# Kernel optimization log

Measured on AMD Instinct MI355X. Metric: run time of the kernel, lower is better.

The kernel has to match this reference:

```python
import jax, jax.numpy as jnp
import numpy as np

DIM = 192
T, H, W = 6, 8, 8
NH = 6
HD = DIM // NH
HW = H * W
N = T * HW
SCALE = HD ** (-0.5)
B_ = 128


def _sine_pos_enc():
    # Faithful port of get_sine_position_encoding(window_size[1:], dim // 2).
    npf = DIM // 2
    ones = jnp.ones((1, H, W), jnp.float32)
    y_embed = jnp.cumsum(ones, axis=1)
    x_embed = jnp.cumsum(ones, axis=2)
    two_pi = 2.0 * np.pi
    y_embed = y_embed / (y_embed[:, -1:, :] + 1e-6) * two_pi
    x_embed = x_embed / (x_embed[:, :, -1:] + 1e-6) * two_pi
    dim_t = jnp.arange(npf, dtype=jnp.float32)
    dim_t = 10000.0 ** (2.0 * jnp.floor(dim_t / 2.0) / npf)
    pos_x = x_embed[:, :, :, None] / dim_t
    pos_y = y_embed[:, :, :, None] / dim_t
    pos_x = jnp.stack((jnp.sin(pos_x[..., 0::2]), jnp.cos(pos_x[..., 1::2])), axis=4).reshape(1, H, W, npf)
    pos_y = jnp.stack((jnp.sin(pos_y[..., 0::2]), jnp.cos(pos_y[..., 1::2])), axis=4).reshape(1, H, W, npf)
    pos = jnp.concatenate((pos_y, pos_x), axis=3)  # (1, H, W, DIM)
    return pos.reshape(1, HW, DIM)


def setup_inputs() -> dict:
    key = jax.random.key(0)
    ks = jax.random.split(key, 6)
    s = 0.02
    return {
        "x": jax.random.normal(ks[0], (B_, N, DIM), jnp.float32),
        "Wqkv": jax.random.normal(ks[1], (3 * DIM, DIM), jnp.float32) * s,
        "Wproj": jax.random.normal(ks[2], (DIM, 2 * DIM), jnp.float32) * s,
        "bproj": jnp.zeros((DIM,), jnp.float32),
        "gamma": jnp.ones((DIM,), jnp.float32),
        "beta": jnp.zeros((DIM,), jnp.float32),
        "W1": jax.random.normal(ks[3], (DIM, DIM), jnp.float32) * s,
        "b1": jnp.zeros((DIM,), jnp.float32),
        "W2": jax.random.normal(ks[4], (DIM, DIM), jnp.float32) * s,
        "b2": jnp.zeros((DIM,), jnp.float32),
    }


def reference(x, Wqkv, Wproj, bproj, gamma, beta, W1, b1, W2, b2):
    b = x.shape[0]
    pos = jnp.tile(_sine_pos_enc(), (1, T, 1))  # (1, N, DIM)
    qkv = (x + pos) @ Wqkv.T                      # (b, N, 3*DIM)
    qkv = qkv.reshape(b, N, 3, NH, HD).transpose(2, 0, 3, 1, 4)
    # temporal chunks: (b, NH, T, HW, HD)
    q = qkv[0].reshape(b, NH, T, HW, HD)
    k = qkv[1].reshape(b, NH, T, HW, HD)
    v = qkv[2].reshape(b, NH, T, HW, HD)
    # all T x T cross-frame attention pairs at once
    scores = jnp.einsum('bhind,bhjmd->ijbhnm', q * SCALE, k)  # (T,T,b,NH,HW,HW)
    attn = jax.nn.softmax(scores, axis=-1)
    o = jnp.einsum('ijbhnm,bhjmd->ijbnhd', attn, v).reshape(T, T, b, HW, DIM)
    # Faithful to torch's x.view(-1, B_, HW, C): raw reinterpretation, not a transpose.
    x_tmp = x.reshape(T, b, HW, DIM)
    xi = jnp.broadcast_to(x_tmp[:, None], (T, T, b, HW, DIM))
    x_att = jnp.concatenate((o, xi), axis=-1)     # (T,T,b,HW,2*DIM)
    y = x_att @ Wproj.T + bproj
    mu = jnp.mean(y, axis=-1, keepdims=True)
    var = jnp.var(y, axis=-1, keepdims=True)
    y = (y - mu) / jnp.sqrt(var + 1e-5) * gamma + beta
    y = jax.nn.gelu(y @ W1.T + b1, approximate=False) @ W2.T + b2
    acc = jnp.sum(y, axis=1)                       # sum over j -> (T,b,HW,DIM)
    x_out = x + acc.transpose(1, 0, 2, 3).reshape(b, N, DIM) / T
    return jnp.concatenate((x, x_out), axis=-1)
```

## Files before the change

### kernel.cpp

```cpp
#include <hip/hip_runtime.h>
#include <cmath>

#define TT   6
#define NB   128
#define DIM  192
#define SCALE 0.17677669529663687f

typedef __attribute__((ext_vector_type(8))) short v8s;
typedef __attribute__((ext_vector_type(4))) float v4f;

__device__ __forceinline__ short f2bf(float f) {
  union { float f; unsigned u; } v; v.f = f;
  unsigned r = v.u + 0x7fffu + ((v.u >> 16) & 1u);
  return (short)(r >> 16);
}

__global__ void prep_kernel(const float* __restrict__ Wqkv, const float* __restrict__ Wproj,
                            const float* __restrict__ W1, const float* __restrict__ W2,
                            short* __restrict__ dWqkv, short* __restrict__ dWproj,
                            short* __restrict__ dW1, short* __restrict__ dW2,
                            float* __restrict__ pos) {
  int idx = blockIdx.x * 256 + threadIdx.x;
  const float* src = nullptr; short* dst = nullptr; int off = 0;
  if (idx < 27648)      { src = Wqkv;  dst = dWqkv;  off = idx; }
  else if (idx < 46080) { src = Wproj; dst = dWproj; off = idx - 27648; }
  else if (idx < 55296) { src = W1;    dst = dW1;    off = idx - 46080; }
  else if (idx < 64512) { src = W2;    dst = dW2;    off = idx - 55296; }
  else if (idx < 67584) {
    int p0 = (idx - 64512) * 4;
    float4 r;
    float* rp = (float*)&r;
#pragma unroll
    for (int jj = 0; jj < 4; jj++) {
      int p = p0 + jj;
      int row = p / 192, c = p - row * 192;
      int e  = (c < 96) ? (row >> 3) : (row & 7);
      int cc = (c < 96) ? c : c - 96;
      int m = cc >> 1;
      float embed = (float)(e + 1) * (6.283185307179586f / 8.000001f);
      float dt = powf(10000.0f, (float)m * (1.0f / 48.0f));
      float ang = embed / dt;
      rp[jj] = (cc & 1) ? cosf(ang) : sinf(ang);
    }
    *(float4*)(pos + p0) = r;
    return;
  } else return;
  const float* s = src + off * 4;
  short4 r;
  r.x = f2bf(s[0]); r.y = f2bf(s[1]); r.z = f2bf(s[2]); r.w = f2bf(s[3]);
  *(short4*)(dst + off * 4) = r;
}

__global__ __launch_bounds__(256) void qkv_kernel(
    const float* __restrict__ x, const float* __restrict__ pos,
    const short* __restrict__ Wqkv_bf,
    short* __restrict__ Qb, short* __restrict__ Kb, short* __restrict__ Vtb) {
  __shared__ short XP[64 * 200];
  int bid = blockIdx.x;
  int xcd = bid & 7, idx = bid >> 3;
  int bq = idx / TT;
  int b = xcd * 16 + bq, t = idx - bq * TT;
  int tid = threadIdx.x, w = tid >> 6, lane = tid & 63;
  int l15 = lane & 15, quad = lane >> 4;
  const float* xrow = x + (size_t)(b * (TT * 64) + t * 64) * DIM;
  for (int c = tid; c < 64 * 24; c += 256) {
    int row = c / 24, col8 = (c - (c / 24) * 24) * 8;
    const float* xs = xrow + row * DIM + col8;
    const float* pp = pos + row * DIM + col8;
    v8s r8;
#pragma unroll
    for (int jj = 0; jj < 8; jj++) r8[jj] = f2bf(xs[jj] + pp[jj]);
    *(v8s*)(XP + row * 200 + col8) = r8;
  }
  __syncthreads();
  const v4f vzero = {0.f, 0.f, 0.f, 0.f};
  size_t obase = (size_t)(b * TT + t) * 64 * DIM;
#pragma unroll
  for (int cti = 0; cti < 9; cti++) {
    int r0 = w * 144 + cti * 16;
    v4f acc[4] = {vzero, vzero, vzero, vzero};
#pragma unroll
    for (int ks = 0; ks < 6; ks++) {
      v8s a = *(const v8s*)(Wqkv_bf + (size_t)(r0 + l15) * 192 + ks * 32 + quad * 8);
#pragma unroll
      for (int nt = 0; nt < 4; nt++) {
        v8s bb = *(const v8s*)(XP + (nt * 16 + l15) * 200 + ks * 32 + quad * 8);
        acc[nt] = __builtin_amdgcn_mfma_f32_16x16x32_bf16(a, bb, acc[nt], 0, 0, 0);
      }
    }
    int R = r0 + quad * 4;
#pragma unroll
    for (int nt = 0; nt < 4; nt++) {
      int hw = nt * 16 + l15;
      if (R < 192) {
        short4 s;
        s.x = f2bf(acc[nt][0] * SCALE); s.y = f2bf(acc[nt][1] * SCALE);
        s.z = f2bf(acc[nt][2] * SCALE); s.w = f2bf(acc[nt][3] * SCALE);
        *(short4*)(Qb + obase + (size_t)hw * 192 + R) = s;
      } else if (R < 384) {
        short4 s;
        s.x = f2bf(acc[nt][0]); s.y = f2bf(acc[nt][1]);
        s.z = f2bf(acc[nt][2]); s.w = f2bf(acc[nt][3]);
        *(short4*)(Kb + obase + (size_t)hw * 192 + (R - 192)) = s;
      } else {
#pragma unroll
        for (int r = 0; r < 4; r++)
          Vtb[obase + (size_t)(R - 384 + r) * 64 + hw] = f2bf(acc[nt][r]);
      }
    }
  }
}

__global__ __launch_bounds__(512, 6) void fused_all(
    const float* __restrict__ x,
    const short* __restrict__ Qb, const short* __restrict__ Kb,
    const short* __restrict__ Vtb,
    const short* __restrict__ Wproj_bf, const short* __restrict__ W1_bf,
    const short* __restrict__ W2_bf,
    const float* __restrict__ bproj, const float* __restrict__ gamma,
    const float* __restrict__ beta, const float* __restrict__ b1,
    const float* __restrict__ b2,
    float* __restrict__ out) {
  __shared__ short SP[64 * 200];
  __shared__ short XI[64 * 200];
  __shared__ float LNp[64][4][2];

  int bid = blockIdx.x;
  int xcd = bid & 7, idx6 = bid >> 3;
  int bq = idx6 / TT;
  int b = xcd * 16 + bq, i = idx6 - bq * TT;

  int tid = threadIdx.x, w = tid >> 6, lane = tid & 63;
  int l15 = lane & 15, quad = lane >> 4;
  int wc = w & 3, wh = w >> 2;
  int cb = wc * 48;
  const v4f vzero = {0.f, 0.f, 0.f, 0.f};

  const float* xi = x + (size_t)(i * NB + b) * 64 * DIM;
  for (int c = tid; c < 64 * 24; c += 512) {
    int row = c / 24, col8 = (c - (c / 24) * 24) * 8;
    const float* xs = xi + row * DIM + col8;
    v8s r8;
#pragma unroll
    for (int jj = 0; jj < 8; jj++) r8[jj] = f2bf(xs[jj]);
    *(v8s*)(XI + row * 200 + col8) = r8;
  }

  const short* Qi = Qb + (size_t)(b * TT + i) * 64 * DIM;
  v8s qa[3];
#pragma unroll
  for (int hh = 0; hh < 3; hh++)
    qa[hh] = *(const v8s*)(Qi + (size_t)(wc * 16 + l15) * 192 + (wh * 3 + hh) * 32 + quad * 8);

  v4f acc[3][2];
#pragma unroll
  for (int cti = 0; cti < 3; cti++)
#pragma unroll
    for (int nt = 0; nt < 2; nt++) acc[cti][nt] = vzero;

  __syncthreads();

  int srcA = l15 + ((lane & 16) << 1);
  int srcB = srcA + 16;
  bool hiq = (lane & 32) != 0;

  for (int j = 0; j < TT; j++) {
    __syncthreads();
    const short* Kj = Kb + (size_t)(b * TT + j) * 64 * DIM;
    const short* Vj = Vtb + (size_t)(b * TT + j) * 64 * DIM;

#pragma unroll
    for (int hh = 0; hh < 3; hh++) {
      int h = wh * 3 + hh;
      v4f S[4];
#pragma unroll
      for (int cta = 0; cta < 4; cta++) {
        v8s akq = *(const v8s*)(Kj + (size_t)(cta * 16 + l15) * 192 + h * 32 + quad * 8);
        S[cta] = __builtin_amdgcn_mfma_f32_16x16x32_bf16(akq, qa[hh], vzero, 0, 0, 0);
      }
      float mx = -1e30f;
#pragma unroll
      for (int cta = 0; cta < 4; cta++)
#pragma unroll
        for (int r = 0; r < 4; r++) mx = fmaxf(mx, S[cta][r]);
      mx = fmaxf(mx, __shfl_xor(mx, 16, 64));
      mx = fmaxf(mx, __shfl_xor(mx, 32, 64));
      float sum = 0.f;
#pragma unroll
      for (int cta = 0; cta < 4; cta++)
#pragma unroll
        for (int r = 0; r < 4; r++) {
          float e = __expf(S[cta][r] - mx);
          S[cta][r] = e; sum += e;
        }
      sum += __shfl_xor(sum, 16, 64);
      sum += __shfl_xor(sum, 32, 64);
      float inv = 1.0f / sum;
      unsigned pk[4][2];
#pragma unroll
      for (int cta = 0; cta < 4; cta++) {
        float a0 = S[cta][0] * inv, a1 = S[cta][1] * inv;
        float a2 = S[cta][2] * inv, a3 = S[cta][3] * inv;
        __asm__("v_cvt_pk_bf16_f32 %0, %1, %2" : "=v"(pk[cta][0]) : "v"(a0), "v"(a1));
        __asm__("v_cvt_pk_bf16_f32 %0, %1, %2" : "=v"(pk[cta][1]) : "v"(a2), "v"(a3));
      }
      unsigned t00 = (unsigned)__shfl((int)pk[0][0], srcA), t10 = (unsigned)__shfl((int)pk[1][0], srcA);
      unsigned t01 = (unsigned)__shfl((int)pk[0][1], srcA), t11 = (unsigned)__shfl((int)pk[1][1], srcA);
      unsigned u00 = (unsigned)__shfl((int)pk[0][0], srcB), u10 = (unsigned)__shfl((int)pk[1][0], srcB);
      unsigned u01 = (unsigned)__shfl((int)pk[0][1], srcB), u11 = (unsigned)__shfl((int)pk[1][1], srcB);
      unsigned s20 = (unsigned)__shfl((int)pk[2][0], srcA), s30 = (unsigned)__shfl((int)pk[3][0], srcA);
      unsigned s21 = (unsigned)__shfl((int)pk[2][1], srcA), s31 = (unsigned)__shfl((int)pk[3][1], srcA);
      unsigned v20 = (unsigned)__shfl((int)pk[2][0], srcB), v30 = (unsigned)__shfl((int)pk[3][0], srcB);
      unsigned v21 = (unsigned)__shfl((int)pk[2][1], srcB), v31 = (unsigned)__shfl((int)pk[3][1], srcB);
      union { unsigned u[4]; v8s v; } B0, B1;
      B0.u[0] = hiq ? t10 : t00;  B0.u[1] = hiq ? t11 : t01;
      B0.u[2] = hiq ? u10 : u00;  B0.u[3] = hiq ? u11 : u01;
      B1.u[0] = hiq ? s30 : s20;  B1.u[1] = hiq ? s31 : s21;
      B1.u[2] = hiq ? v30 : v20;  B1.u[3] = hiq ? v31 : v21;
#pragma unroll
      for (int ct2 = 0; ct2 < 2; ct2++) {
        v8s av0 = *(const v8s*)(Vj + (size_t)(h * 32 + ct2 * 16 + l15) * 64 + quad * 8);
        v8s av1 = *(const v8s*)(Vj + (size_t)(h * 32 + ct2 * 16 + l15) * 64 + 32 + quad * 8);
        v4f o = __builtin_amdgcn_mfma_f32_16x16x32_bf16(av0, B0.v, vzero, 0, 0, 0);
        o = __builtin_amdgcn_mfma_f32_16x16x32_bf16(av1, B1.v, o, 0, 0, 0);
        short4 s;
        s.x = f2bf(o[0]); s.y = f2bf(o[1]); s.z = f2bf(o[2]); s.w = f2bf(o[3]);
        *(short4*)(&SP[(wc * 16 + l15) * 200 + h * 32 + ct2 * 16 + quad * 4]) = s;
      }
    }
    __syncthreads();

    v4f y1[3][2];
#pragma unroll
    for (int cti = 0; cti < 3; cti++)
#pragma unroll
      for (int nt = 0; nt < 2; nt++) y1[cti][nt] = vzero;
#pragma unroll
    for (int ks = 0; ks < 6; ks++) {
      v8s bo[2];
#pragma unroll
      for (int nt = 0; nt < 2; nt++)
        bo[nt] = *(const v8s*)(SP + (wh * 32 + nt * 16 + l15) * 200 + ks * 32 + quad * 8);
#pragma unroll
      for (int cti = 0; cti < 3; cti++) {
        v8s a = *(const v8s*)(Wproj_bf + (size_t)(cb + cti * 16 + l15) * 384 + ks * 32 + quad * 8);
#pragma unroll
        for (int nt = 0; nt < 2; nt++)
          y1[cti][nt] = __builtin_amdgcn_mfma_f32_16x16x32_bf16(a, bo[nt], y1[cti][nt], 0, 0, 0);
      }
    }
#pragma unroll
    for (int ks = 0; ks < 6; ks++) {
      v8s bxi[2];
#pragma unroll
      for (int nt = 0; nt < 2; nt++)
        bxi[nt] = *(const v8s*)(XI + (wh * 32 + nt * 16 + l15) * 200 + ks * 32 + quad * 8);
#pragma unroll
      for (int cti = 0; cti < 3; cti++) {
        v8s a = *(const v8s*)(Wproj_bf + (size_t)(cb + cti * 16 + l15) * 384 + 192 + ks * 32 + quad * 8);
#pragma unroll
        for (int nt = 0; nt < 2; nt++)
          y1[cti][nt] = __builtin_amdgcn_mfma_f32_16x16x32_bf16(a, bxi[nt], y1[cti][nt], 0, 0, 0);
      }
    }
#pragma unroll
    for (int cti = 0; cti < 3; cti++) {
      float4 bp4 = *(const float4*)(bproj + cb + cti * 16 + quad * 4);
#pragma unroll
      for (int nt = 0; nt < 2; nt++) {
        y1[cti][nt][0] += bp4.x; y1[cti][nt][1] += bp4.y;
        y1[cti][nt][2] += bp4.z; y1[cti][nt][3] += bp4.w;
      }
    }
#pragma unroll
    for (int nt = 0; nt < 2; nt++) {
      float s1 = 0.f, s2 = 0.f;
#pragma unroll
      for (int cti = 0; cti < 3; cti++)
#pragma unroll
        for (int r = 0; r < 4; r++) { float v = y1[cti][nt][r]; s1 += v; s2 += v * v; }
      s1 += __shfl_xor(s1, 16, 64); s2 += __shfl_xor(s2, 16, 64);
      s1 += __shfl_xor(s1, 32, 64); s2 += __shfl_xor(s2, 32, 64);
      if (quad == 0) {
        LNp[wh * 32 + nt * 16 + l15][wc][0] = s1;
        LNp[wh * 32 + nt * 16 + l15][wc][1] = s2;
      }
    }
    __syncthreads();
    float mu[2], rs[2];
#pragma unroll
    for (int nt = 0; nt < 2; nt++) {
      int row = wh * 32 + nt * 16 + l15;
      float s1 = 0.f, s2 = 0.f;
#pragma unroll
      for (int ww = 0; ww < 4; ww++) { s1 += LNp[row][ww][0]; s2 += LNp[row][ww][1]; }
      float m = s1 * (1.0f / 192.0f);
      mu[nt] = m; rs[nt] = rsqrtf(s2 * (1.0f / 192.0f) - m * m + 1e-5f);
    }
#pragma unroll
    for (int cti = 0; cti < 3; cti++) {
      float4 g4 = *(const float4*)(gamma + cb + cti * 16 + quad * 4);
      float4 be4 = *(const float4*)(beta + cb + cti * 16 + quad * 4);
#pragma unroll
      for (int nt = 0; nt < 2; nt++) {
        short4 s;
        s.x = f2bf((y1[cti][nt][0] - mu[nt]) * rs[nt] * g4.x + be4.x);
        s.y = f2bf((y1[cti][nt][1] - mu[nt]) * rs[nt] * g4.y + be4.y);
        s.z = f2bf((y1[cti][nt][2] - mu[nt]) * rs[nt] * g4.z + be4.z);
        s.w = f2bf((y1[cti][nt][3] - mu[nt]) * rs[nt] * g4.w + be4.w);
        *(short4*)(&SP[(wh * 32 + nt * 16 + l15) * 200 + cb + cti * 16 + quad * 4]) = s;
      }
    }
    __syncthreads();

    v4f y2[3][2];
#pragma unroll
    for (int cti = 0; cti < 3; cti++)
#pragma unroll
      for (int nt = 0; nt < 2; nt++) y2[cti][nt] = vzero;
#pragma unroll
    for (int ks = 0; ks < 6; ks++) {
      v8s bh[2];
#pragma unroll
      for (int nt = 0; nt < 2; nt++)
        bh[nt] = *(const v8s*)(SP + (wh * 32 + nt * 16 + l15) * 200 + ks * 32 + quad * 8);
#pragma unroll
      for (int cti = 0; cti < 3; cti++) {
        v8s a = *(const v8s*)(W1_bf + (size_t)(cb + cti * 16 + l15) * 192 + ks * 32 + quad * 8);
#pragma unroll
        for (int nt = 0; nt < 2; nt++)
          y2[cti][nt] = __builtin_amdgcn_mfma_f32_16x16x32_bf16(a, bh[nt], y2[cti][nt], 0, 0, 0);
      }
    }
    __syncthreads();
#pragma unroll
    for (int cti = 0; cti < 3; cti++) {
      float4 b14 = *(const float4*)(b1 + cb + cti * 16 + quad * 4);
#pragma unroll
      for (int nt = 0; nt < 2; nt++) {
        float vv[4] = {y2[cti][nt][0] + b14.x, y2[cti][nt][1] + b14.y,
                       y2[cti][nt][2] + b14.z, y2[cti][nt][3] + b14.w};
        short sv[4];
#pragma unroll
        for (int r = 0; r < 4; r++) {
          float v = vv[r];
          float t = 0.79788456080286536f * (v + 0.044715f * v * v * v);
          float e = __expf(2.0f * t);
          float th = 1.0f - 2.0f / (e + 1.0f);
          sv[r] = f2bf(0.5f * v * (1.0f + th));
        }
        short4 s;
        s.x = sv[0]; s.y = sv[1]; s.z = sv[2]; s.w = sv[3];
        *(short4*)(&SP[(wh * 32 + nt * 16 + l15) * 200 + cb + cti * 16 + quad * 4]) = s;
      }
    }
    __syncthreads();

#pragma unroll
    for (int ks = 0; ks < 6; ks++) {
      v8s bh[2];
#pragma unroll
      for (int nt = 0; nt < 2; nt++)
        bh[nt] = *(const v8s*)(SP + (wh * 32 + nt * 16 + l15) * 200 + ks * 32 + quad * 8);
#pragma unroll
      for (int cti = 0; cti < 3; cti++) {
        v8s a = *(const v8s*)(W2_bf + (size_t)(cb + cti * 16 + l15) * 192 + ks * 32 + quad * 8);
#pragma unroll
        for (int nt = 0; nt < 2; nt++)
          acc[cti][nt] = __builtin_amdgcn_mfma_f32_16x16x32_bf16(a, bh[nt], acc[cti][nt], 0, 0, 0);
      }
    }
  }

  float* SPf = (float*)SP;
#pragma unroll
  for (int pass = 0; pass < 2; pass++) {
    __syncthreads();
    if (wh == pass) {
#pragma unroll
      for (int cti = 0; cti < 3; cti++)
#pragma unroll
        for (int nt = 0; nt < 2; nt++) {
          float4 o4;
          o4.x = acc[cti][nt][0] * (1.0f / 6.0f);
          o4.y = acc[cti][nt][1] * (1.0f / 6.0f);
          o4.z = acc[cti][nt][2] * (1.0f / 6.0f);
          o4.w = acc[cti][nt][3] * (1.0f / 6.0f);
          *(float4*)(&SPf[(nt * 16 + l15) * 196 + cb + cti * 16 + quad * 4]) = o4;
        }
    }
    __syncthreads();
    for (int c = tid; c < 1536; c += 512) {
      int r32 = c / 48, col4 = (c - r32 * 48) * 4;
      int row = pass * 32 + r32;
      size_t nrow = (size_t)b * 384 + (size_t)i * 64 + row;
      float4 xv = *(const float4*)(x + nrow * DIM + col4);
      float4 b24 = *(const float4*)(b2 + col4);
      float4 av = *(const float4*)(&SPf[r32 * 196 + col4]);
      float4 o4;
      o4.x = xv.x + av.x + b24.x;
      o4.y = xv.y + av.y + b24.y;
      o4.z = xv.z + av.z + b24.z;
      o4.w = xv.w + av.w + b24.w;
      *(float4*)(out + nrow * 384 + col4) = xv;
      *(float4*)(out + nrow * 384 + 192 + col4) = o4;
    }
  }
}

extern "C" void kernel_launch(void* const* d_in, const int* in_sizes, int n_in,
                              void* d_out, int out_size, void* d_ws, size_t ws_size,
                              hipStream_t stream) {
  (void)in_sizes; (void)n_in; (void)out_size; (void)ws_size;
  const float* x     = (const float*)d_in[0];
  const float* Wqkv  = (const float*)d_in[1];
  const float* Wproj = (const float*)d_in[2];
  const float* bproj = (const float*)d_in[3];
  const float* gamma = (const float*)d_in[4];
  const float* beta  = (const float*)d_in[5];
  const float* W1    = (const float*)d_in[6];
  const float* b1    = (const float*)d_in[7];
  const float* W2    = (const float*)d_in[8];
  const float* b2    = (const float*)d_in[9];
  float* out = (float*)d_out;

  short* Wqkv_bf  = (short*)d_ws;
  short* Wproj_bf = Wqkv_bf + 110592;
  short* W1_bf    = Wproj_bf + 73728;
  short* W2_bf    = W1_bf + 36864;
  float* pos_f    = (float*)(W2_bf + 36864);
  short* Qb       = (short*)(pos_f + 12288);
  short* Kb       = Qb + 9437184;
  short* Vtb      = Kb + 9437184;

  prep_kernel<<<dim3(264), dim3(256), 0, stream>>>(
      Wqkv, Wproj, W1, W2, Wqkv_bf, Wproj_bf, W1_bf, W2_bf, pos_f);
  qkv_kernel<<<dim3(TT * NB), dim3(256), 0, stream>>>(x, pos_f, Wqkv_bf, Qb, Kb, Vtb);
  fused_all<<<dim3(TT * NB), dim3(512), 0, stream>>>(
      x, Qb, Kb, Vtb, Wproj_bf, W1_bf, W2_bf, bproj, gamma, beta, b1, b2, out);
}
```

Measured before the change: 632.6 us.

## Hoist x-half projection out of j loop and route softmax probs through LDS

The Wproj times x_i half of the projection does not depend on j, so it is now computed once before the loop and used to seed each iteration's accumulator, removing repeated MFMA work. Softmax probabilities are transposed through a per-wave LDS scratch buffer instead of sixteen lane shuffles and selects. The attention for j+1 moves to the end of iteration j, and a separate GELU buffer removes one block barrier. Launch bounds drop from 6 to 4 waves per SIMD, which lowers the occupancy target, while the extra registers and LDS may cut residency.

```diff
diff --git a/kernel.cpp b/kernel.cpp
--- a/kernel.cpp
+++ b/kernel.cpp
@@ -13,6 +13,9 @@
   union { float f; unsigned u; } v; v.f = f;
   unsigned r = v.u + 0x7fffu + ((v.u >> 16) & 1u);
   return (short)(r >> 16);
+}
+__device__ __forceinline__ void fence() {
+  __asm__ volatile("s_waitcnt lgkmcnt(0)" ::: "memory");
 }
 
 __global__ void prep_kernel(const float* __restrict__ Wqkv, const float* __restrict__ Wproj,
@@ -111,7 +114,7 @@
   }
 }
 
-__global__ __launch_bounds__(512, 6) void fused_all(
+__global__ __launch_bounds__(512, 4) void fused_all(
     const float* __restrict__ x,
     const short* __restrict__ Qb, const short* __restrict__ Kb,
     const short* __restrict__ Vtb,
@@ -122,7 +125,8 @@
     const float* __restrict__ b2,
     float* __restrict__ out) {
   __shared__ short SP[64 * 200];
-  __shared__ short XI[64 * 200];
+  __shared__ short HB[64 * 200];
+  __shared__ short Pl[8][16 * 72];
   __shared__ float LNp[64][4][2];
 
   int bid = blockIdx.x;
@@ -143,7 +147,7 @@
     v8s r8;
 #pragma unroll
     for (int jj = 0; jj < 8; jj++) r8[jj] = f2bf(xs[jj]);
-    *(v8s*)(XI + row * 200 + col8) = r8;
+    *(v8s*)(SP + row * 200 + col8) = r8;
   }
 
   const short* Qi = Qb + (size_t)(b * TT + i) * 64 * DIM;
@@ -160,15 +164,28 @@
 
   __syncthreads();
 
-  int srcA = l15 + ((lane & 16) << 1);
-  int srcB = srcA + 16;
-  bool hiq = (lane & 32) != 0;
-
-  for (int j = 0; j < TT; j++) {
-    __syncthreads();
-    const short* Kj = Kb + (size_t)(b * TT + j) * 64 * DIM;
-    const short* Vj = Vtb + (size_t)(b * TT + j) * 64 * DIM;
-
+  v4f y1x[3][2];
+#pragma unroll
+  for (int cti = 0; cti < 3; cti++)
+#pragma unroll
+    for (int nt = 0; nt < 2; nt++) y1x[cti][nt] = vzero;
+#pragma unroll
+  for (int ks = 0; ks < 6; ks++) {
+    v8s bxi[2];
+#pragma unroll
+    for (int nt = 0; nt < 2; nt++)
+      bxi[nt] = *(const v8s*)(SP + (wh * 32 + nt * 16 + l15) * 200 + ks * 32 + quad * 8);
+#pragma unroll
+    for (int cti = 0; cti < 3; cti++) {
+      v8s a = *(const v8s*)(Wproj_bf + (size_t)(cb + cti * 16 + l15) * 384 + 192 + ks * 32 + quad * 8);
+#pragma unroll
+      for (int nt = 0; nt < 2; nt++)
+        y1x[cti][nt] = __builtin_amdgcn_mfma_f32_16x16x32_bf16(a, bxi[nt], y1x[cti][nt], 0, 0, 0);
+    }
+  }
+  __syncthreads();
+
+  auto attn = [&](const short* Kj, const short* Vj) {
 #pragma unroll
     for (int hh = 0; hh < 3; hh++) {
       int h = wh * 3 + hh;
@@ -196,45 +213,42 @@
       sum += __shfl_xor(sum, 16, 64);
       sum += __shfl_xor(sum, 32, 64);
       float inv = 1.0f / sum;
-      unsigned pk[4][2];
 #pragma unroll
       for (int cta = 0; cta < 4; cta++) {
-        float a0 = S[cta][0] * inv, a1 = S[cta][1] * inv;
-        float a2 = S[cta][2] * inv, a3 = S[cta][3] * inv;
-        __asm__("v_cvt_pk_bf16_f32 %0, %1, %2" : "=v"(pk[cta][0]) : "v"(a0), "v"(a1));
-        __asm__("v_cvt_pk_bf16_f32 %0, %1, %2" : "=v"(pk[cta][1]) : "v"(a2), "v"(a3));
-      }
-      unsigned t00 = (unsigned)__shfl((int)pk[0][0], srcA), t10 = (unsigned)__shfl((int)pk[1][0], srcA);
-      unsigned t01 = (unsigned)__shfl((int)pk[0][1], srcA), t11 = (unsigned)__shfl((int)pk[1][1], srcA);
-      unsigned u00 = (unsigned)__shfl((int)pk[0][0], srcB), u10 = (unsigned)__shfl((int)pk[1][0], srcB);
-      unsigned u01 = (unsigned)__shfl((int)pk[0][1], srcB), u11 = (unsigned)__shfl((int)pk[1][1], srcB);
-      unsigned s20 = (unsigned)__shfl((int)pk[2][0], srcA), s30 = (unsigned)__shfl((int)pk[3][0], srcA);
-      unsigned s21 = (unsigned)__shfl((int)pk[2][1], srcA), s31 = (unsigned)__shfl((int)pk[3][1], srcA);
-      unsigned v20 = (unsigned)__shfl((int)pk[2][0], srcB), v30 = (unsigned)__shfl((int)pk[3][0], srcB);
-      unsigned v21 = (unsigned)__shfl((int)pk[2][1], srcB), v31 = (unsigned)__shfl((int)pk[3][1], srcB);
-      union { unsigned u[4]; v8s v; } B0, B1;
-      B0.u[0] = hiq ? t10 : t00;  B0.u[1] = hiq ? t11 : t01;
-      B0.u[2] = hiq ? u10 : u00;  B0.u[3] = hiq ? u11 : u01;
-      B1.u[0] = hiq ? s30 : s20;  B1.u[1] = hiq ? s31 : s21;
-      B1.u[2] = hiq ? v30 : v20;  B1.u[3] = hiq ? v31 : v21;
+        short4 s;
+        s.x = f2bf(S[cta][0] * inv); s.y = f2bf(S[cta][1] * inv);
+        s.z = f2bf(S[cta][2] * inv); s.w = f2bf(S[cta][3] * inv);
+        *(short4*)(&Pl[w][l15 * 72 + cta * 16 + quad * 4]) = s;
+      }
+      fence();
+      v8s bp0 = *(const v8s*)(&Pl[w][l15 * 72 + quad * 8]);
+      v8s bp1 = *(const v8s*)(&Pl[w][l15 * 72 + 32 + quad * 8]);
 #pragma unroll
       for (int ct2 = 0; ct2 < 2; ct2++) {
         v8s av0 = *(const v8s*)(Vj + (size_t)(h * 32 + ct2 * 16 + l15) * 64 + quad * 8);
         v8s av1 = *(const v8s*)(Vj + (size_t)(h * 32 + ct2 * 16 + l15) * 64 + 32 + quad * 8);
-        v4f o = __builtin_amdgcn_mfma_f32_16x16x32_bf16(av0, B0.v, vzero, 0, 0, 0);
-        o = __builtin_amdgcn_mfma_f32_16x16x32_bf16(av1, B1.v, o, 0, 0, 0);
+        v4f o = __builtin_amdgcn_mfma_f32_16x16x32_bf16(av0, bp0, vzero, 0, 0, 0);
+        o = __builtin_amdgcn_mfma_f32_16x16x32_bf16(av1, bp1, o, 0, 0, 0);
         short4 s;
         s.x = f2bf(o[0]); s.y = f2bf(o[1]); s.z = f2bf(o[2]); s.w = f2bf(o[3]);
         *(short4*)(&SP[(wc * 16 + l15) * 200 + h * 32 + ct2 * 16 + quad * 4]) = s;
       }
-    }
+      fence();
+    }
+  };
+
+  const short* KB0 = Kb + (size_t)(b * TT) * 64 * DIM;
+  const short* VB0 = Vtb + (size_t)(b * TT) * 64 * DIM;
+  attn(KB0, VB0);
+
+  for (int j = 0; j < TT; j++) {
     __syncthreads();
 
     v4f y1[3][2];
 #pragma unroll
     for (int cti = 0; cti < 3; cti++)
 #pragma unroll
-      for (int nt = 0; nt < 2; nt++) y1[cti][nt] = vzero;
+      for (int nt = 0; nt < 2; nt++) y1[cti][nt] = y1x[cti][nt];
 #pragma unroll
     for (int ks = 0; ks < 6; ks++) {
       v8s bo[2];
@@ -247,20 +261,6 @@
 #pragma unroll
         for (int nt = 0; nt < 2; nt++)
           y1[cti][nt] = __builtin_amdgcn_mfma_f32_16x16x32_bf16(a, bo[nt], y1[cti][nt], 0, 0, 0);
-      }
-    }
-#pragma unroll
-    for (int ks = 0; ks < 6; ks++) {
-      v8s bxi[2];
-#pragma unroll
-      for (int nt = 0; nt < 2; nt++)
-        bxi[nt] = *(const v8s*)(XI + (wh * 32 + nt * 16 + l15) * 200 + ks * 32 + quad * 8);
-#pragma unroll
-      for (int cti = 0; cti < 3; cti++) {
-        v8s a = *(const v8s*)(Wproj_bf + (size_t)(cb + cti * 16 + l15) * 384 + 192 + ks * 32 + quad * 8);
-#pragma unroll
-        for (int nt = 0; nt < 2; nt++)
-          y1[cti][nt] = __builtin_amdgcn_mfma_f32_16x16x32_bf16(a, bxi[nt], y1[cti][nt], 0, 0, 0);
       }
     }
 #pragma unroll
@@ -332,7 +332,6 @@
           y2[cti][nt] = __builtin_amdgcn_mfma_f32_16x16x32_bf16(a, bh[nt], y2[cti][nt], 0, 0, 0);
       }
     }
-    __syncthreads();
 #pragma unroll
     for (int cti = 0; cti < 3; cti++) {
       float4 b14 = *(const float4*)(b1 + cb + cti * 16 + quad * 4);
@@ -351,7 +350,7 @@
         }
         short4 s;
         s.x = sv[0]; s.y = sv[1]; s.z = sv[2]; s.w = sv[3];
-        *(short4*)(&SP[(wh * 32 + nt * 16 + l15) * 200 + cb + cti * 16 + quad * 4]) = s;
+        *(short4*)(&HB[(wh * 32 + nt * 16 + l15) * 200 + cb + cti * 16 + quad * 4]) = s;
       }
     }
     __syncthreads();
@@ -361,7 +360,7 @@
       v8s bh[2];
 #pragma unroll
       for (int nt = 0; nt < 2; nt++)
-        bh[nt] = *(const v8s*)(SP + (wh * 32 + nt * 16 + l15) * 200 + ks * 32 + quad * 8);
+        bh[nt] = *(const v8s*)(HB + (wh * 32 + nt * 16 + l15) * 200 + ks * 32 + quad * 8);
 #pragma unroll
       for (int cti = 0; cti < 3; cti++) {
         v8s a = *(const v8s*)(W2_bf + (size_t)(cb + cti * 16 + l15) * 192 + ks * 32 + quad * 8);
@@ -369,6 +368,10 @@
         for (int nt = 0; nt < 2; nt++)
           acc[cti][nt] = __builtin_amdgcn_mfma_f32_16x16x32_bf16(a, bh[nt], acc[cti][nt], 0, 0, 0);
       }
+    }
+    if (j < TT - 1) {
+      attn(Kb + (size_t)(b * TT + j + 1) * 64 * DIM,
+           Vtb + (size_t)(b * TT + j + 1) * 64 * DIM);
     }
   }
 
```

Result: slower. 930.5 us (+47.1%).
